# Kernel optimization log

Measured on AMD Instinct MI355X. Metric: run time of the kernel, lower is better.

Reference implementation:

```python
import jax, jax.numpy as jnp
import numpy as np

K = 3
PAD = 1
STRIDE = 1


def _conv2d(x, w, b):
    out = jax.lax.conv_general_dilated(
        x, w, window_strides=(STRIDE, STRIDE),
        padding=[(PAD, PAD), (PAD, PAD)],
        dimension_numbers=("NCHW", "OIHW", "NCHW"))
    return out + b[None, :, None, None]


def setup_inputs() -> dict:
    key = jax.random.key(0)
    ks = jax.random.split(key, 6)
    B, C, H, W, O = 4, 64, 128, 128, 64
    x = jax.random.normal(ks[0], (B, C, H, W), dtype=jnp.float32)
    # small-scale offset/modulator weights so sampled offsets stay O(1) pixels
    offset_w = jax.random.normal(ks[1], (2 * K * K, C, K, K), dtype=jnp.float32) * 0.02
    offset_b = jax.random.normal(ks[2], (2 * K * K,), dtype=jnp.float32) * 0.02
    mod_w = jax.random.normal(ks[3], (K * K, C, K, K), dtype=jnp.float32) * 0.02
    mod_b = jax.random.normal(ks[4], (K * K,), dtype=jnp.float32) * 0.02
    weight = jax.random.normal(ks[5], (O, C, K, K), dtype=jnp.float32) * 0.05
    return {"x": x, "offset_w": offset_w, "offset_b": offset_b,
            "mod_w": mod_w, "mod_b": mod_b, "weight": weight}


def _deform_conv(x, offset, mask, weight):
    # torchvision deform_conv2d v2 semantics, zero padding outside the image.
    B, C, H, W = x.shape
    K2 = K * K
    Ho, Wo = offset.shape[2], offset.shape[3]
    dy = offset[:, 0::2]  # [B,K2,Ho,Wo] vertical offsets
    dx = offset[:, 1::2]  # [B,K2,Ho,Wo] horizontal offsets
    ky = jnp.repeat(jnp.arange(K), K).astype(x.dtype)   # kernel row per tap
    kx = jnp.tile(jnp.arange(K), K).astype(x.dtype)     # kernel col per tap
    oy = (jnp.arange(Ho) * STRIDE - PAD).astype(x.dtype)
    ox = (jnp.arange(Wo) * STRIDE - PAD).astype(x.dtype)
    py = oy[None, None, :, None] + ky[None, :, None, None] + dy  # [B,K2,Ho,Wo]
    px = ox[None, None, None, :] + kx[None, :, None, None] + dx

    y0 = jnp.floor(py)
    x0 = jnp.floor(px)
    wy1 = py - y0  # bilinear weights toward the +1 corner
    wx1 = px - x0
    y0i = y0.astype(jnp.int32)
    x0i = x0.astype(jnp.int32)

    xf = x.reshape(B, C, H * W)

    def gather(yc, xc, wgt):
        valid = ((yc >= 0) & (yc < H) & (xc >= 0) & (xc < W)).astype(x.dtype)
        idx = jnp.clip(yc, 0, H - 1) * W + jnp.clip(xc, 0, W - 1)  # [B,K2,Ho,Wo]
        flat = idx.reshape(B, 1, -1)
        g = jnp.take_along_axis(xf, jnp.broadcast_to(flat, (B, C, flat.shape[-1])), axis=2)
        g = g.reshape(B, C, K2, Ho, Wo)
        return g * (wgt * valid)[:, None]

    samp = (gather(y0i,     x0i,     (1 - wy1) * (1 - wx1))
            + gather(y0i,     x0i + 1, (1 - wy1) * wx1)
            + gather(y0i + 1, x0i,     wy1 * (1 - wx1))
            + gather(y0i + 1, x0i + 1, wy1 * wx1))  # [B,C,K2,Ho,Wo]

    wr = weight.reshape(weight.shape[0], C, K2)
    return jnp.einsum("ock,bckhw->bohw", wr, samp * mask[:, None])


def reference(x, offset_w, offset_b, mod_w, mod_b, weight):
    offset = _conv2d(x, offset_w, offset_b)
    mask = 2.0 * jax.nn.sigmoid(_conv2d(x, mod_w, mod_b))
    return _deform_conv(x, offset, mask, weight)
```

## Files before the change

### kernel.cpp

```cpp
#include <hip/hip_runtime.h>
#include <hip/hip_bf16.h>
#include <math.h>

typedef unsigned short u16;
typedef unsigned int   u32;
typedef __attribute__((ext_vector_type(8))) short short8;
typedef __attribute__((ext_vector_type(4))) float f32x4;

#define B_  4
#define C_  64
#define H_  128
#define W_  128
#define O_  64
#define HW_ (H_ * W_)

__device__ __forceinline__ u16 f2bf(float f) {
    __hip_bfloat16 h = __float2bfloat16(f);
    u16 u; __builtin_memcpy(&u, &h, 2); return u;
}
__device__ __forceinline__ float bf2f(u16 u) {
    return __uint_as_float((u32)u << 16);
}
__device__ __forceinline__ u32 pkbf(float lo, float hi) {
    return ((u32)f2bf(hi) << 16) | (u32)f2bf(lo);
}
__device__ __forceinline__ float bflo(u32 v) { return __uint_as_float(v << 16); }
__device__ __forceinline__ float bfhi(u32 v) { return __uint_as_float(v & 0xffff0000u); }

__device__ __forceinline__ uint4 interp8(
    uint4 c00, uint4 c01, uint4 c10, uint4 c11,
    float wtx, float wty, float wtz, float wtw)
{
    const u32* q00 = (const u32*)&c00;
    const u32* q01 = (const u32*)&c01;
    const u32* q10 = (const u32*)&c10;
    const u32* q11 = (const u32*)&c11;
    u32 bw[4];
#pragma unroll
    for (int q = 0; q < 4; ++q) {
        float slo = bflo(q00[q]) * wtx;
        slo = fmaf(bflo(q01[q]), wty, slo);
        slo = fmaf(bflo(q10[q]), wtz, slo);
        slo = fmaf(bflo(q11[q]), wtw, slo);
        float shi = bfhi(q00[q]) * wtx;
        shi = fmaf(bfhi(q01[q]), wty, shi);
        shi = fmaf(bfhi(q10[q]), wtz, shi);
        shi = fmaf(bfhi(q11[q]), wtw, shi);
        bw[q] = pkbf(slo, shi);
    }
    uint4 v; __builtin_memcpy(&v, bw, 16);
    return v;
}

__global__ __launch_bounds__(256) void prep(
    const float* __restrict__ x, const float* __restrict__ weight,
    const float* __restrict__ ow, const float* __restrict__ mw,
    u16* __restrict__ xt, u16* __restrict__ Wb, u16* __restrict__ OWb)
{
    int i = blockIdx.x, t = threadIdx.x;
    if (i < 1024) {
        __shared__ float tile[64][65];
        int lb = i >> 8;
        int pix0 = (i & 255) << 6;
        const float* xb = x + ((size_t)lb << 20);
#pragma unroll
        for (int it = 0; it < 16; ++it) {
            int e = it * 256 + t;
            int c = e >> 6, pl = e & 63;
            tile[c][pl] = xb[((size_t)c << 14) + pix0 + pl];
        }
        __syncthreads();
        u16* xo = xt + ((((size_t)lb << 14) + pix0) << 6);
#pragma unroll
        for (int it = 0; it < 16; ++it) {
            int e = it * 256 + t;
            int c = e & 63, pl = e >> 6;
            xo[((size_t)pl << 6) + c] = f2bf(tile[c][pl]);
        }
    } else {
        int e = (i - 1024) * 256 + t;
        if (e < 36864) {
            int j = e & 7, ln = (e >> 3) & 63;
            int ks = (e >> 9) % 18, ot = e / 9216;
            int o = ot * 16 + (ln & 15);
            int kidx = ks * 32 + ((ln >> 4) << 3) + j;
            int k = kidx >> 6, c = kidx & 63;
            Wb[e] = f2bf(weight[((size_t)(o * 64 + c)) * 9 + k]);
        } else {
            int e2 = e - 36864;
            int j = e2 & 7, ln = (e2 >> 3) & 63;
            int ks = (e2 >> 9) % 18, ot = e2 / 9216;
            int o = ot * 16 + (ln & 15);
            int kidx = ks * 32 + ((ln >> 4) << 3) + j;
            int k = kidx >> 6, c = kidx & 63;
            float v = 0.0f;
            if (o < 18)      v = ow[((size_t)(o * 64 + c)) * 9 + k];
            else if (o < 27) v = mw[((size_t)((o - 18) * 64 + c)) * 9 + k];
            OWb[e2] = f2bf(v);
        }
    }
}

__global__ __launch_bounds__(256, 6) void fused_dcn(
    const u16* __restrict__ xt,
    const u16* __restrict__ Wb, const u16* __restrict__ OWb,
    const float* __restrict__ ob, const float* __restrict__ mb,
    float* __restrict__ out)
{
    __shared__ __align__(16) u16 S[16][576];
    __shared__ float   param[27][16];
    __shared__ __align__(16) int4    pwp[144];
    __shared__ __align__(16) ushort4 pww[144];

    const int t = threadIdx.x;
    const int lane = t & 63;
    const int wv = t >> 6;

    int bid0 = blockIdx.x;
    const int bid = (bid0 & 7) * 512 + (bid0 >> 3);
    const int lb = bid >> 10;
    const int pix0 = (bid & 1023) << 4;
    const int h  = pix0 >> 7;
    const int w0 = pix0 & 127;

    const u16* xtb = xt + ((size_t)lb << 20);
    const char* xb8 = (const char*)xtb;

#pragma unroll
    for (int i = 0; i < 4; ++i) {
        int e = i * 256 + t;
        int u = e >> 3, oct = e & 7;
        int k = u >> 4, pixl = u & 15;
        int ky = k / 3, kx = k - 3 * ky;
        int y = h - 1 + ky, xx = w0 + pixl - 1 + kx;
        bool valid = ((unsigned)y < 128u) && ((unsigned)xx < 128u);
        int idx = ((y & 127) << 7) + (xx & 127);
        uint4 v = *(const uint4*)(xtb + ((size_t)idx << 6) + (oct << 3));
        v.x = valid ? v.x : 0u;
        v.y = valid ? v.y : 0u;
        v.z = valid ? v.z : 0u;
        v.w = valid ? v.w : 0u;
        *(uint4*)&S[pixl][k * 64 + ((oct ^ (pixl & 7)) << 3)] = v;
    }
    if (t < 128) {
        int e = 1024 + t;
        int u = e >> 3, oct = e & 7;
        int pixl = u & 15;
        int y = h + 1;
        int xx = w0 + pixl - 1 + 2;
        bool valid = ((unsigned)y < 128u) && ((unsigned)xx < 128u);
        int idx = ((y & 127) << 7) + (xx & 127);
        uint4 v = *(const uint4*)(xtb + ((size_t)idx << 6) + (oct << 3));
        v.x = valid ? v.x : 0u;
        v.y = valid ? v.y : 0u;
        v.z = valid ? v.z : 0u;
        v.w = valid ? v.w : 0u;
        *(uint4*)&S[pixl][8 * 64 + ((oct ^ (pixl & 7)) << 3)] = v;
    }
    __syncthreads();

    if (wv < 2) {
        f32x4 k1 = {0.f, 0.f, 0.f, 0.f};
        int brow = lane & 15;
        int hi = lane >> 4;
        int swz = (brow & 7) << 3;
#pragma unroll
        for (int ks = 0; ks < 18; ++ks) {
            short8 a = ((const short8*)OWb)[(wv * 18 + ks) * 64 + lane];
            int coff = ((ks & 1) << 5) + (hi << 3);
            short8 bf = *(const short8*)&S[brow][(ks >> 1) * 64 + (coff ^ swz)];
            k1 = __builtin_amdgcn_mfma_f32_16x16x32_bf16(a, bf, k1, 0, 0, 0);
        }
#pragma unroll
        for (int r = 0; r < 4; ++r) {
            int oc = wv * 16 + (hi << 2) + r;
            if (oc < 18) {
                param[oc][brow] = k1[r] + ob[oc];
            } else if (oc < 27) {
                float s = k1[r] + mb[oc - 18];
                param[oc][brow] = 2.0f / (1.0f + __expf(-s));
            }
        }
    }
    __syncthreads();

    if (t < 144) {
        int tap = t >> 4, pixl = t & 15;
        int ky = tap / 3, kx = tap - 3 * ky;
        float dy = param[2 * tap][pixl];
        float dx = param[2 * tap + 1][pixl];
        float m  = param[18 + tap][pixl];
        float py = (float)(h - 1 + ky) + dy;
        float px = (float)(w0 + pixl - 1 + kx) + dx;
        float y0f = floorf(py), x0f = floorf(px);
        float fy = py - y0f, fx = px - x0f;
        int y0 = (int)y0f, x0 = (int)x0f;
        int y1 = y0 + 1, x1 = x0 + 1;
        bool vy0 = (unsigned)y0 < (unsigned)H_;
        bool vy1 = (unsigned)y1 < (unsigned)H_;
        bool vx0 = (unsigned)x0 < (unsigned)W_;
        bool vx1 = (unsigned)x1 < (unsigned)W_;
        float w00 = (1.f - fy) * (1.f - fx) * m; if (!(vy0 && vx0)) w00 = 0.f;
        float w01 = (1.f - fy) * fx          * m; if (!(vy0 && vx1)) w01 = 0.f;
        float w10 = fy * (1.f - fx)          * m; if (!(vy1 && vx0)) w10 = 0.f;
        float w11 = fy * fx                   * m; if (!(vy1 && vx1)) w11 = 0.f;
        int y0c = min(max(y0, 0), H_ - 1);
        int y1c = min(max(y1, 0), H_ - 1);
        int x0c = min(max(x0, 0), W_ - 1);
        int x1c = min(max(x1, 0), W_ - 1);
        pwp[t] = make_int4(((y0c << 7) + x0c) << 7, ((y0c << 7) + x1c) << 7,
                           ((y1c << 7) + x0c) << 7, ((y1c << 7) + x1c) << 7);
        pww[t] = make_ushort4(f2bf(w00), f2bf(w01), f2bf(w10), f2bf(w11));
    }
    __syncthreads();

#pragma unroll
    for (int ii = 0; ii < 2; ++ii) {
        int e0 = ii * 512 + t;
        int e1 = e0 + 256;
        int u0 = e0 >> 3, o0 = e0 & 7;
        int u1 = e1 >> 3, o1 = e1 & 7;
        int4    ofs0 = pwp[u0]; ushort4 wq0 = pww[u0];
        int4    ofs1 = pwp[u1]; ushort4 wq1 = pww[u1];
        uint4 a00 = *(const uint4*)(xb8 + ofs0.x + (o0 << 4));
        uint4 a01 = *(const uint4*)(xb8 + ofs0.y + (o0 << 4));
        uint4 a10 = *(const uint4*)(xb8 + ofs0.z + (o0 << 4));
        uint4 a11 = *(const uint4*)(xb8 + ofs0.w + (o0 << 4));
        uint4 b00 = *(const uint4*)(xb8 + ofs1.x + (o1 << 4));
        uint4 b01 = *(const uint4*)(xb8 + ofs1.y + (o1 << 4));
        uint4 b10 = *(const uint4*)(xb8 + ofs1.z + (o1 << 4));
        uint4 b11 = *(const uint4*)(xb8 + ofs1.w + (o1 << 4));
        __builtin_amdgcn_sched_barrier(0);
        {
            int k = u0 >> 4, pixl = u0 & 15;
            uint4 v = interp8(a00, a01, a10, a11,
                              bf2f(wq0.x), bf2f(wq0.y), bf2f(wq0.z), bf2f(wq0.w));
            *(uint4*)&S[pixl][k * 64 + ((o0 ^ (pixl & 7)) << 3)] = v;
        }
        {
            int k = u1 >> 4, pixl = u1 & 15;
            uint4 v = interp8(b00, b01, b10, b11,
                              bf2f(wq1.x), bf2f(wq1.y), bf2f(wq1.z), bf2f(wq1.w));
            *(uint4*)&S[pixl][k * 64 + ((o1 ^ (pixl & 7)) << 3)] = v;
        }
    }
    if (t < 128) {
        int e = 1024 + t;
        int u = e >> 3, oct = e & 7;
        int pixl = u & 15;
        int4    ofs = pwp[u]; ushort4 wq = pww[u];
        uint4 c00 = *(const uint4*)(xb8 + ofs.x + (oct << 4));
        uint4 c01 = *(const uint4*)(xb8 + ofs.y + (oct << 4));
        uint4 c10 = *(const uint4*)(xb8 + ofs.z + (oct << 4));
        uint4 c11 = *(const uint4*)(xb8 + ofs.w + (oct << 4));
        uint4 v = interp8(c00, c01, c10, c11,
                          bf2f(wq.x), bf2f(wq.y), bf2f(wq.z), bf2f(wq.w));
        *(uint4*)&S[pixl][8 * 64 + ((oct ^ (pixl & 7)) << 3)] = v;
    }
    __syncthreads();

    {
        f32x4 acc = {0.f, 0.f, 0.f, 0.f};
        int brow = lane & 15;
        int hi = lane >> 4;
        int swz = (brow & 7) << 3;
#pragma unroll
        for (int ks = 0; ks < 18; ++ks) {
            int coff = ((ks & 1) << 5) + (hi << 3);
            short8 bfr = *(const short8*)&S[brow][(ks >> 1) * 64 + (coff ^ swz)];
            short8 a = ((const short8*)Wb)[(wv * 18 + ks) * 64 + lane];
            acc = __builtin_amdgcn_mfma_f32_16x16x32_bf16(a, bfr, acc, 0, 0, 0);
        }
        float* op = out + ((size_t)lb << 20) + pix0;
#pragma unroll
        for (int r = 0; r < 4; ++r) {
            int o = wv * 16 + (hi << 2) + r;
            op[((size_t)o << 14) + brow] = acc[r];
        }
    }
}

extern "C" void kernel_launch(void* const* d_in, const int* in_sizes, int n_in,
                              void* d_out, int out_size, void* d_ws, size_t ws_size,
                              hipStream_t stream)
{
    const float* x        = (const float*)d_in[0];
    const float* offset_w = (const float*)d_in[1];
    const float* offset_b = (const float*)d_in[2];
    const float* mod_w    = (const float*)d_in[3];
    const float* mod_b    = (const float*)d_in[4];
    const float* weight   = (const float*)d_in[5];
    float* out = (float*)d_out;

    u16* Wb  = (u16*)d_ws;
    u16* OWb = Wb + 36864;
    u16* xt  = OWb + 18432;

    prep<<<1240, 256, 0, stream>>>(x, weight, offset_w, mod_w, xt, Wb, OWb);
    fused_dcn<<<4096, 256, 0, stream>>>(xt, Wb, OWb, offset_b, mod_b, out);
}
```

Baseline: 43.99 us.

## Vectorize prep transpose, compact gather offsets, split MFMA accumulators, raise occupancy

The prep transpose now uses float4 loads and ushort4 stores in place of scalar accesses. Bilinear corner offsets are stored in LDS as 16-bit pixel indices instead of int4 byte offsets, which halves that buffer at the cost of a shift per load. Both MFMA loops use two independent accumulators to break the serial dependency chain. The launch-bounds occupancy hint goes from 6 to 7 waves, which may force register spills.

New measurement: 44.29 us. About the same (+0.7%).

```diff
diff --git a/kernel.cpp b/kernel.cpp
--- a/kernel.cpp
+++ b/kernel.cpp
@@ -64,18 +64,29 @@
         int pix0 = (i & 255) << 6;
         const float* xb = x + ((size_t)lb << 20);
 #pragma unroll
-        for (int it = 0; it < 16; ++it) {
+        for (int it = 0; it < 4; ++it) {
             int e = it * 256 + t;
-            int c = e >> 6, pl = e & 63;
-            tile[c][pl] = xb[((size_t)c << 14) + pix0 + pl];
+            int c = e >> 4;
+            int pl4 = (e & 15) << 2;
+            float4 v = *(const float4*)&xb[((size_t)c << 14) + pix0 + pl4];
+            tile[c][pl4 + 0] = v.x;
+            tile[c][pl4 + 1] = v.y;
+            tile[c][pl4 + 2] = v.z;
+            tile[c][pl4 + 3] = v.w;
         }
         __syncthreads();
         u16* xo = xt + ((((size_t)lb << 14) + pix0) << 6);
 #pragma unroll
-        for (int it = 0; it < 16; ++it) {
+        for (int it = 0; it < 4; ++it) {
             int e = it * 256 + t;
-            int c = e & 63, pl = e >> 6;
-            xo[((size_t)pl << 6) + c] = f2bf(tile[c][pl]);
+            int c4 = (e & 15) << 2;
+            int pl = e >> 4;
+            ushort4 v;
+            v.x = f2bf(tile[c4 + 0][pl]);
+            v.y = f2bf(tile[c4 + 1][pl]);
+            v.z = f2bf(tile[c4 + 2][pl]);
+            v.w = f2bf(tile[c4 + 3][pl]);
+            *(ushort4*)&xo[((size_t)pl << 6) + c4] = v;
         }
     } else {
         int e = (i - 1024) * 256 + t;
@@ -101,7 +112,7 @@
     }
 }
 
-__global__ __launch_bounds__(256, 6) void fused_dcn(
+__global__ __launch_bounds__(256, 7) void fused_dcn(
     const u16* __restrict__ xt,
     const u16* __restrict__ Wb, const u16* __restrict__ OWb,
     const float* __restrict__ ob, const float* __restrict__ mb,
@@ -109,8 +120,8 @@
 {
     __shared__ __align__(16) u16 S[16][576];
     __shared__ float   param[27][16];
-    __shared__ __align__(16) int4    pwp[144];
-    __shared__ __align__(16) ushort4 pww[144];
+    __shared__ __align__(8) ushort4 pwp[144];
+    __shared__ __align__(8) ushort4 pww[144];
 
     const int t = threadIdx.x;
     const int lane = t & 63;
@@ -160,24 +171,29 @@
     __syncthreads();
 
     if (wv < 2) {
-        f32x4 k1 = {0.f, 0.f, 0.f, 0.f};
+        f32x4 k1a = {0.f, 0.f, 0.f, 0.f};
+        f32x4 k1b = {0.f, 0.f, 0.f, 0.f};
         int brow = lane & 15;
         int hi = lane >> 4;
         int swz = (brow & 7) << 3;
 #pragma unroll
-        for (int ks = 0; ks < 18; ++ks) {
-            short8 a = ((const short8*)OWb)[(wv * 18 + ks) * 64 + lane];
-            int coff = ((ks & 1) << 5) + (hi << 3);
-            short8 bf = *(const short8*)&S[brow][(ks >> 1) * 64 + (coff ^ swz)];
-            k1 = __builtin_amdgcn_mfma_f32_16x16x32_bf16(a, bf, k1, 0, 0, 0);
+        for (int kp = 0; kp < 9; ++kp) {
+            int ks0 = kp * 2, ks1 = kp * 2 + 1;
+            short8 a0 = ((const short8*)OWb)[(wv * 18 + ks0) * 64 + lane];
+            short8 a1 = ((const short8*)OWb)[(wv * 18 + ks1) * 64 + lane];
+            short8 b0 = *(const short8*)&S[brow][kp * 64 + ((hi << 3) ^ swz)];
+            short8 b1 = *(const short8*)&S[brow][kp * 64 + ((32 + (hi << 3)) ^ swz)];
+            k1a = __builtin_amdgcn_mfma_f32_16x16x32_bf16(a0, b0, k1a, 0, 0, 0);
+            k1b = __builtin_amdgcn_mfma_f32_16x16x32_bf16(a1, b1, k1b, 0, 0, 0);
         }
 #pragma unroll
         for (int r = 0; r < 4; ++r) {
             int oc = wv * 16 + (hi << 2) + r;
+            float v = k1a[r] + k1b[r];
             if (oc < 18) {
-                param[oc][brow] = k1[r] + ob[oc];
+                param[oc][brow] = v + ob[oc];
             } else if (oc < 27) {
-                float s = k1[r] + mb[oc - 18];
+                float s = v + mb[oc - 18];
                 param[oc][brow] = 2.0f / (1.0f + __expf(-s));
             }
         }
@@ -208,8 +224,8 @@
         int y1c = min(max(y1, 0), H_ - 1);
         int x0c = min(max(x0, 0), W_ - 1);
         int x1c = min(max(x1, 0), W_ - 1);
-        pwp[t] = make_int4(((y0c << 7) + x0c) << 7, ((y0c << 7) + x1c) << 7,
-                           ((y1c << 7) + x0c) << 7, ((y1c << 7) + x1c) << 7);
+        pwp[t] = make_ushort4((u16)((y0c << 7) + x0c), (u16)((y0c << 7) + x1c),
+                              (u16)((y1c << 7) + x0c), (u16)((y1c << 7) + x1c));
         pww[t] = make_ushort4(f2bf(w00), f2bf(w01), f2bf(w10), f2bf(w11));
     }
     __syncthreads();
@@ -220,16 +236,17 @@
         int e1 = e0 + 256;
         int u0 = e0 >> 3, o0 = e0 & 7;
         int u1 = e1 >> 3, o1 = e1 & 7;
-        int4    ofs0 = pwp[u0]; ushort4 wq0 = pww[u0];
-        int4    ofs1 = pwp[u1]; ushort4 wq1 = pww[u1];
-        uint4 a00 = *(const uint4*)(xb8 + ofs0.x + (o0 << 4));
-        uint4 a01 = *(const uint4*)(xb8 + ofs0.y + (o0 << 4));
-        uint4 a10 = *(const uint4*)(xb8 + ofs0.z + (o0 << 4));
-        uint4 a11 = *(const uint4*)(xb8 + ofs0.w + (o0 << 4));
-        uint4 b00 = *(const uint4*)(xb8 + ofs1.x + (o1 << 4));
-        uint4 b01 = *(const uint4*)(xb8 + ofs1.y + (o1 << 4));
-        uint4 b10 = *(const uint4*)(xb8 + ofs1.z + (o1 << 4));
-        uint4 b11 = *(const uint4*)(xb8 + ofs1.w + (o1 << 4));
+        ushort4 pp0 = pwp[u0]; ushort4 wq0 = pww[u0];
+        ushort4 pp1 = pwp[u1]; ushort4 wq1 = pww[u1];
+        int co0 = o0 << 4, co1 = o1 << 4;
+        uint4 a00 = *(const uint4*)(xb8 + ((int)pp0.x << 7) + co0);
+        uint4 a01 = *(const uint4*)(xb8 + ((int)pp0.y << 7) + co0);
+        uint4 a10 = *(const uint4*)(xb8 + ((int)pp0.z << 7) + co0);
+        uint4 a11 = *(const uint4*)(xb8 + ((int)pp0.w << 7) + co0);
+        uint4 b00 = *(const uint4*)(xb8 + ((int)pp1.x << 7) + co1);
+        uint4 b01 = *(const uint4*)(xb8 + ((int)pp1.y << 7) + co1);
+        uint4 b10 = *(const uint4*)(xb8 + ((int)pp1.z << 7) + co1);
+        uint4 b11 = *(const uint4*)(xb8 + ((int)pp1.w << 7) + co1);
         __builtin_amdgcn_sched_barrier(0);
         {
             int k = u0 >> 4, pixl = u0 & 15;
@@ -248,11 +265,12 @@
         int e = 1024 + t;
         int u = e >> 3, oct = e & 7;
         int pixl = u & 15;
-        int4    ofs = pwp[u]; ushort4 wq = pww[u];
-        uint4 c00 = *(const uint4*)(xb8 + ofs.x + (oct << 4));
-        uint4 c01 = *(const uint4*)(xb8 + ofs.y + (oct << 4));
-        uint4 c10 = *(const uint4*)(xb8 + ofs.z + (oct << 4));
-        uint4 c11 = *(const uint4*)(xb8 + ofs.w + (oct << 4));
+        ushort4 pp = pwp[u]; ushort4 wq = pww[u];
+        int co = oct << 4;
+        uint4 c00 = *(const uint4*)(xb8 + ((int)pp.x << 7) + co);
+        uint4 c01 = *(const uint4*)(xb8 + ((int)pp.y << 7) + co);
+        uint4 c10 = *(const uint4*)(xb8 + ((int)pp.z << 7) + co);
+        uint4 c11 = *(const uint4*)(xb8 + ((int)pp.w << 7) + co);
         uint4 v = interp8(c00, c01, c10, c11,
                           bf2f(wq.x), bf2f(wq.y), bf2f(wq.z), bf2f(wq.w));
         *(uint4*)&S[pixl][8 * 64 + ((oct ^ (pixl & 7)) << 3)] = v;
@@ -260,22 +278,26 @@
     __syncthreads();
 
     {
-        f32x4 acc = {0.f, 0.f, 0.f, 0.f};
+        f32x4 acca = {0.f, 0.f, 0.f, 0.f};
+        f32x4 accb = {0.f, 0.f, 0.f, 0.f};
         int brow = lane & 15;
         int hi = lane >> 4;
         int swz = (brow & 7) << 3;
 #pragma unroll
-        for (int ks = 0; ks < 18; ++ks) {
-            int coff = ((ks & 1) << 5) + (hi << 3);
-            short8 bfr = *(const short8*)&S[brow][(ks >> 1) * 64 + (coff ^ swz)];
-            short8 a = ((const short8*)Wb)[(wv * 18 + ks) * 64 + lane];
-            acc = __builtin_amdgcn_mfma_f32_16x16x32_bf16(a, bfr, acc, 0, 0, 0);
+        for (int kp = 0; kp < 9; ++kp) {
+            int ks0 = kp * 2, ks1 = kp * 2 + 1;
+            short8 b0 = *(const short8*)&S[brow][kp * 64 + ((hi << 3) ^ swz)];
+            short8 b1 = *(const short8*)&S[brow][kp * 64 + ((32 + (hi << 3)) ^ swz)];
+            short8 a0 = ((const short8*)Wb)[(wv * 18 + ks0) * 64 + lane];
+            short8 a1 = ((const short8*)Wb)[(wv * 18 + ks1) * 64 + lane];
+            acca = __builtin_amdgcn_mfma_f32_16x16x32_bf16(a0, b0, acca, 0, 0, 0);
+            accb = __builtin_amdgcn_mfma_f32_16x16x32_bf16(a1, b1, accb, 0, 0, 0);
         }
         float* op = out + ((size_t)lb << 20) + pix0;
 #pragma unroll
         for (int r = 0; r < 4; ++r) {
             int o = wv * 16 + (hi << 2) + r;
-            op[((size_t)o << 14) + brow] = acc[r];
+            op[((size_t)o << 14) + brow] = acca[r] + accb[r];
         }
     }
 }
```
